# Optimization experiments

Hardware: AMD Instinct MI355X
Metric: run time of the kernel (lower is better)

## Reference

```python
import jax, jax.numpy as jnp
import numpy as np

B, S, D = 16, 1024, 512
H, DH = 8, 64  # heads, dim_head


def setup_inputs() -> dict:
    key = jax.random.key(0)
    ks = jax.random.split(key, 7)
    x = jax.random.normal(ks[0], (B, S, D), dtype=jnp.float32)
    # variable sequence lengths in [1, S]
    seq_lens = jnp.maximum(jax.random.randint(ks[1], (B,), 0, S + 1), 1).astype(jnp.int32)
    w_std = 0.02
    Wq = jax.random.normal(ks[2], (D, D), dtype=jnp.float32) * w_std
    Wk = jax.random.normal(ks[3], (D, D), dtype=jnp.float32) * w_std
    Wv = jax.random.normal(ks[4], (D, D), dtype=jnp.float32) * w_std
    Wo = jax.random.normal(ks[5], (D, D), dtype=jnp.float32) * w_std
    bo = jnp.zeros((D,), dtype=jnp.float32)
    return {"x": x, "seq_lens": seq_lens, "Wq": Wq, "Wk": Wk, "Wv": Wv, "Wo": Wo, "bo": bo}


def reference(x, seq_lens, Wq, Wk, Wv, Wo, bo):
    # x: [B, S, D] padded ragged batch; seq_lens: [B] valid token counts.
    # Equivalent to the per-batch SDPA loop over jagged sequences: attention
    # is computed only among the valid tokens of each sequence.
    scale = DH ** -0.5
    q = (x @ Wq).reshape(B, S, H, DH)
    k = (x @ Wk).reshape(B, S, H, DH)
    v = (x @ Wv).reshape(B, S, H, DH)
    scores = jnp.einsum('bqhd,bkhd->bhqk', q, k) * scale  # [B,H,S,S]
    valid = jnp.arange(S)[None, :] < seq_lens[:, None]     # [B,S] token mask
    neg_inf = jnp.finfo(scores.dtype).min
    scores = jnp.where(valid[:, None, None, :], scores, neg_inf)
    attn = jax.nn.softmax(scores, axis=-1)
    out = jnp.einsum('bhqk,bkhd->bqhd', attn, v).reshape(B, S, D)
    out = out @ Wo + bo  # to_out Linear (dropout=0 / eval)
    return out * valid[:, :, None]  # zero padded query positions
```

## Files before the change

### kernel.cpp

```cpp
#include <hip/hip_runtime.h>
#include <hip/hip_bf16.h>

typedef __bf16 bf16_t;
typedef __attribute__((ext_vector_type(4))) __bf16 bf16x4;
typedef __attribute__((ext_vector_type(8))) __bf16 bf16x8;
typedef __attribute__((ext_vector_type(4))) float f32x4;

#define MFMA16(a, b, c) __builtin_amdgcn_mfma_f32_16x16x32_bf16((a), (b), (c), 0, 0, 0)

#define BB 16
#define SS 1024
#define DD 512
#define HH 8
#define DH 64
#define NTOK (BB * SS)
#define QSCALE 0.18033688f

typedef const __attribute__((address_space(1))) void gas_void;
typedef __attribute__((address_space(3))) void las_void;

__device__ __forceinline__ void async_cp16(const void* g, void* l) {
    __builtin_amdgcn_global_load_lds((gas_void*)g, (las_void*)l, 16, 0, 0);
}

__device__ __forceinline__ bf16x8 frag_ld(const char* sm, int row, int kk, int g) {
    int r7 = row & 7;
    int base = row * 128 + ((g & 1) << 3);
    int c0 = ((kk << 2) + (g >> 1)) ^ r7;
    int c1 = ((kk << 2) + 2 + (g >> 1)) ^ r7;
    bf16x4 lo = *(const bf16x4*)(sm + base + (c0 << 4));
    bf16x4 hi = *(const bf16x4*)(sm + base + (c1 << 4));
    return __builtin_shufflevector(lo, hi, 0, 1, 2, 3, 4, 5, 6, 7);
}

__device__ __forceinline__ bf16x8 fragl(const char* sm, int idx, int l) {
    return *(const bf16x8*)(sm + (idx * 64 + l) * 16);
}

__global__ __launch_bounds__(256) void cast_x_k(const float* __restrict__ x,
                                                bf16_t* __restrict__ xb, int n4) {
    int i = blockIdx.x * 256 + threadIdx.x;
    if (i < n4) {
        float4 v = ((const float4*)x)[i];
        bf16x4 o;
        o[0] = (bf16_t)v.x; o[1] = (bf16_t)v.y; o[2] = (bf16_t)v.z; o[3] = (bf16_t)v.w;
        *(bf16x4*)(xb + (size_t)i * 4) = o;
    }
}

__global__ __launch_bounds__(256) void transpose_w_k(const float* __restrict__ W0,
                                                     const float* __restrict__ W1,
                                                     const float* __restrict__ W2,
                                                     const float* __restrict__ W3,
                                                     bf16_t* __restrict__ Wt) {
    __shared__ float t[32][33];
    int z = blockIdx.z;
    const float* W = (z == 0) ? W0 : (z == 1) ? W1 : (z == 2) ? W2 : W3;
    bf16_t* out = Wt + (size_t)z * DD * DD;
    int n0 = blockIdx.x * 32, k0 = blockIdx.y * 32;
    int tx = threadIdx.x, ty = threadIdx.y;
#pragma unroll
    for (int i = 0; i < 32; i += 8)
        t[ty + i][tx] = W[(size_t)(k0 + ty + i) * DD + n0 + tx];
    __syncthreads();
#pragma unroll
    for (int i = 0; i < 32; i += 8)
        out[(size_t)(n0 + ty + i) * DD + k0 + tx] = (bf16_t)t[tx][ty + i];
}

__global__ void build_q_k(const int* __restrict__ sl, ushort* __restrict__ items,
                          int* __restrict__ meta) {
    int l = threadIdx.x;
    __shared__ int s_b[BB], s_cnt[BB], s_start[BB];
    if (l < BB) {
        int len = sl[l];
        int rank = 0;
        for (int j = 0; j < BB; ++j) {
            int lj = sl[j];
            if (lj > len || (lj == len && j < l)) ++rank;
        }
        s_b[rank] = l;
        s_cnt[rank] = ((len + 63) >> 6) * HH;
    }
    __syncthreads();
    if (l < BB) {
        int st = 0;
        for (int j = 0; j < l; ++j) st += s_cnt[j];
        s_start[l] = st;
        if (l == BB - 1) { meta[0] = st + s_cnt[l]; meta[1] = 0; }
    }
    __syncthreads();
    if (l < BB) {
        int b = s_b[l], st = s_start[l], c = s_cnt[l];
        int nq = c >> 3;
        for (int i = 0; i < c; ++i) {
            int h = i / nq, qt = i - h * nq;
            items[st + i] = (ushort)((((b << 3) | h) << 4) | qt);
        }
    }
}

template <int MODE>
__global__ __launch_bounds__(256) void gemm_k(const bf16_t* __restrict__ A,
                                              const bf16_t* __restrict__ WtBase,
                                              bf16_t* __restrict__ oQ,
                                              bf16_t* __restrict__ oK,
                                              bf16_t* __restrict__ oVt,
                                              float* __restrict__ oO,
                                              const float* __restrict__ bo,
                                              const int* __restrict__ seq_lens) {
    __shared__ __align__(16) char smem[32768];
    char* smA = smem;
    char* smB = smem + 16384;
    const int tid = threadIdx.x;
    const int l = tid & 63, w = tid >> 6;
    const int lr = l & 15, g = l >> 4;
    const int bm = blockIdx.x, bn = blockIdx.y;
    const int z = (MODE == 0) ? blockIdx.z : 3;
    const bf16_t* Wt = WtBase + (size_t)z * DD * DD;
    const int row0 = bm * 128;
    const int col0 = bn * 128;
    const int wm = (w >> 1) * 64, wn = (w & 1) * 64;

    const int bb = row0 >> 10, s0 = row0 & 1023;
    const int len = seq_lens[bb];

    if (MODE == 0) {
        if (s0 >= ((len + 63) & ~63)) return;
    } else {
        if (s0 >= len) {
#pragma unroll
            for (int i = 0; i < 4; ++i) {
                int mrow = row0 + wm + i * 16 + g * 4;
#pragma unroll
                for (int j = 0; j < 4; ++j) {
                    int n = col0 + wn + j * 16 + lr;
#pragma unroll
                    for (int r = 0; r < 4; ++r)
                        oO[(size_t)(mrow + r) * DD + n] = 0.f;
                }
            }
            return;
        }
    }

    f32x4 acc[4][4] = {};

    for (int kt = 0; kt < 8; ++kt) {
        const int k0 = kt * 64;
        __syncthreads();
#pragma unroll
        for (int it = 0; it < 4; ++it) {
            int cl = it * 256 + tid;
            int m = cl >> 3, p = cl & 7, c = p ^ (m & 7);
            async_cp16(A + (size_t)(row0 + m) * DD + k0 + c * 8, smA + cl * 16);
        }
#pragma unroll
        for (int it = 0; it < 4; ++it) {
            int cl = it * 256 + tid;
            int m = cl >> 3, p = cl & 7, c = p ^ (m & 7);
            async_cp16(Wt + (size_t)(col0 + m) * DD + k0 + c * 8, smB + cl * 16);
        }
        __syncthreads();
#pragma unroll
        for (int kk = 0; kk < 2; ++kk) {
            bf16x8 af[4], bfr[4];
#pragma unroll
            for (int i = 0; i < 4; ++i) af[i] = frag_ld(smA, wm + i * 16 + lr, kk, g);
#pragma unroll
            for (int j = 0; j < 4; ++j) bfr[j] = frag_ld(smB, wn + j * 16 + lr, kk, g);
#pragma unroll
            for (int i = 0; i < 4; ++i)
#pragma unroll
                for (int j = 0; j < 4; ++j)
                    acc[i][j] = MFMA16(af[i], bfr[j], acc[i][j]);
        }
    }

    if (MODE == 0) {
        __syncthreads();
        char* tl = smem;
        const float sc = (z == 0) ? QSCALE : 1.f;
#pragma unroll
        for (int i = 0; i < 4; ++i)
#pragma unroll
            for (int j = 0; j < 4; ++j)
#pragma unroll
                for (int r = 0; r < 4; ++r) {
                    int s = wm + i * 16 + g * 4 + r;
                    int n = wn + j * 16 + lr;
                    int nb = 2 * n;
                    int byte = s * 256 + ((((nb >> 4) ^ (s & 7)) << 4) | (nb & 15));
                    *(bf16_t*)(tl + byte) = (bf16_t)(acc[i][j][r] * sc);
                }
        __syncthreads();
        const int b = bb;
        if (z < 2) {
            bf16_t* dst = (z == 0) ? oQ : oK;
#pragma unroll
            for (int c8 = 0; c8 < 8; ++c8) {
                int combo = c8 * 4 + w;
                int kk = combo & 1, t = (combo >> 1) & 7, hl = combo >> 4;
                int s = 16 * t + lr;
                bf16x4 pr[2];
#pragma unroll
                for (int jj = 0; jj < 2; ++jj) {
                    int nb = 128 * hl + 64 * kk + 32 * jj + 8 * g;
                    int byte = s * 256 + ((((nb >> 4) ^ (s & 7)) << 4) | (nb & 15));
                    pr[jj] = *(const bf16x4*)(tl + byte);
                }
                bf16x8 v = __builtin_shufflevector(pr[0], pr[1], 0, 1, 2, 3, 4, 5, 6, 7);
                int bhh = b * 8 + (col0 >> 6) + hl;
                int tg = (s0 >> 4) + t;
                *(bf16x8*)(dst + (((size_t)bhh * 64 + tg) * 2 + kk) * 512 + l * 8) = v;
            }
        } else {
#pragma unroll
            for (int c8 = 0; c8 < 8; ++c8) {
                int combo = c8 * 4 + w;
                int kk = combo & 1, dt = (combo >> 1) & 3;
                int st = (combo >> 3) & 1, hl = (combo >> 4) & 1;
                bf16x8 v;
#pragma unroll
                for (int j = 0; j < 8; ++j) {
                    int s = 64 * st + 32 * kk + 16 * (j >> 2) + 4 * g + (j & 3);
                    int n = 64 * hl + 16 * dt + lr;
                    int nb = 2 * n;
                    int byte = s * 256 + ((((nb >> 4) ^ (s & 7)) << 4) | (nb & 15));
                    v[j] = *(const bf16_t*)(tl + byte);
                }
                int bhh = b * 8 + (col0 >> 6) + hl;
                int stg = (s0 >> 6) + st;
                *(bf16x8*)(oVt + ((((size_t)bhh * 16 + stg) * 4 + dt) * 2 + kk) * 512 +
                           l * 8) = v;
            }
        }
    } else {
        const bool fullv = (s0 + 128 <= len);
#pragma unroll
        for (int i = 0; i < 4; ++i) {
            int mrow = row0 + wm + i * 16 + g * 4;
#pragma unroll
            for (int j = 0; j < 4; ++j) {
                int n = col0 + wn + j * 16 + lr;
                float bias = bo[n];
                if (fullv) {
#pragma unroll
                    for (int r = 0; r < 4; ++r)
                        oO[(size_t)(mrow + r) * DD + n] = acc[i][j][r] + bias;
                } else {
#pragma unroll
                    for (int r = 0; r < 4; ++r) {
                        int m = mrow + r;
                        int s = m & 1023;
                        oO[(size_t)m * DD + n] = (s < len) ? (acc[i][j][r] + bias) : 0.f;
                    }
                }
            }
        }
    }
}

__global__ __launch_bounds__(256) void attn_k(const bf16_t* __restrict__ Qf,
                                              const bf16_t* __restrict__ Kf,
                                              const bf16_t* __restrict__ Vf,
                                              bf16_t* __restrict__ O,
                                              const int* __restrict__ seq_lens,
                                              const ushort* __restrict__ items,
                                              int* __restrict__ meta) {
    __shared__ __align__(16) char smem[32768];
    __shared__ int s_item;
    const int tid = threadIdx.x, l = tid & 63, w = tid >> 6;
    const int lr = l & 15, g = l >> 4;
    const int nitems = meta[0];
    int* cursor = meta + 1;

    for (;;) {
        if (tid == 0) s_item = atomicAdd(cursor, 1);
        __syncthreads();
        const int ii = s_item;
        if (ii >= nitems) return;
        const int itv = items[ii];
        const int qt = itv & 15, bh = itv >> 4;
        const int b = bh >> 3, h = bh & 7;
        const int len = seq_lens[b];
        const int q0 = qt * 64 + w * 16;

        const bf16_t* kfb = Kf + (size_t)bh * 65536;
        const bf16_t* vfb = Vf + (size_t)bh * 65536;

        bf16x8 bq[2];
        {
            size_t tb = ((size_t)bh * 64 + (q0 >> 4)) * 2;
            bq[0] = *(const bf16x8*)(Qf + (tb + 0) * 512 + l * 8);
            bq[1] = *(const bf16x8*)(Qf + (tb + 1) * 512 + l * 8);
        }

        f32x4 oacc[4] = {};
        float mrun = -1e30f, lpart = 0.f;

        const int nkt = (len + 63) >> 6;

        auto stage = [&](int buf, int kti) {
            char* smK = smem + buf * 16384;
            char* smV = smK + 8192;
            const bf16_t* ks = kfb + kti * 4096;
            const bf16_t* vs = vfb + kti * 4096;
            async_cp16(ks + tid * 8, smK + tid * 16);
            async_cp16(ks + (256 + tid) * 8, smK + (256 + tid) * 16);
            async_cp16(vs + tid * 8, smV + tid * 16);
            async_cp16(vs + (256 + tid) * 8, smV + (256 + tid) * 16);
        };

        stage(0, 0);
        int cur = 0;

        for (int kt = 0; kt < nkt; ++kt) {
            const int key0 = kt * 64;
            asm volatile("s_waitcnt vmcnt(0)" ::: "memory");
            __builtin_amdgcn_s_barrier();
            if (kt + 1 < nkt) stage(cur ^ 1, kt + 1);
            const char* smK = smem + cur * 16384;
            const char* smV = smK + 8192;

            f32x4 pacc[4] = {};
            __builtin_amdgcn_s_setprio(1);
#pragma unroll
            for (int nt = 0; nt < 4; ++nt) {
                bf16x8 ak0 = fragl(smK, nt * 2 + 0, l);
                bf16x8 ak1 = fragl(smK, nt * 2 + 1, l);
                pacc[nt] = MFMA16(ak0, bq[0], pacc[nt]);
                pacc[nt] = MFMA16(ak1, bq[1], pacc[nt]);
            }
            __builtin_amdgcn_s_setprio(0);

            const bool full = (key0 + 64 <= len);

            float mloc = -1e30f;
            if (full) {
#pragma unroll
                for (int nt = 0; nt < 4; ++nt)
#pragma unroll
                    for (int r = 0; r < 4; ++r) mloc = fmaxf(mloc, pacc[nt][r]);
            } else {
#pragma unroll
                for (int nt = 0; nt < 4; ++nt)
#pragma unroll
                    for (int r = 0; r < 4; ++r) {
                        int kg = key0 + nt * 16 + 4 * g + r;
                        float s = (kg < len) ? pacc[nt][r] : -1e30f;
                        pacc[nt][r] = s;
                        mloc = fmaxf(mloc, s);
                    }
            }
            mloc = fmaxf(mloc, __shfl_xor(mloc, 16, 64));
            mloc = fmaxf(mloc, __shfl_xor(mloc, 32, 64));

            if (!__all(mloc <= mrun + 8.f)) {
                float mn = fmaxf(mrun, mloc);
                float corr = __builtin_amdgcn_exp2f(mrun - mn);
                mrun = mn;
                lpart *= corr;
                float cb[4];
#pragma unroll
                for (int r = 0; r < 4; ++r) cb[r] = __shfl(corr, 4 * g + r, 64);
#pragma unroll
                for (int dt = 0; dt < 4; ++dt)
#pragma unroll
                    for (int r = 0; r < 4; ++r) oacc[dt][r] *= cb[r];
            }

            float ls = 0.f;
#pragma unroll
            for (int nt = 0; nt < 4; ++nt)
#pragma unroll
                for (int r = 0; r < 4; ++r) {
                    float p = __builtin_amdgcn_exp2f(pacc[nt][r] - mrun);
                    pacc[nt][r] = p;
                    ls += p;
                }
            lpart += ls;

            bf16x8 pa[2];
#pragma unroll
            for (int kf = 0; kf < 2; ++kf)
#pragma unroll
                for (int j = 0; j < 8; ++j)
                    pa[kf][j] = (bf16_t)pacc[2 * kf + (j >> 2)][j & 3];
            __builtin_amdgcn_s_setprio(1);
#pragma unroll
            for (int kf = 0; kf < 2; ++kf)
#pragma unroll
                for (int dt = 0; dt < 4; ++dt) {
                    bf16x8 bv = fragl(smV, dt * 2 + kf, l);
                    oacc[dt] = MFMA16(pa[kf], bv, oacc[dt]);
                }
            __builtin_amdgcn_s_setprio(0);
            cur ^= 1;
        }

        {
            float lt = lpart;
            lt += __shfl_xor(lt, 16, 64);
            lt += __shfl_xor(lt, 32, 64);
#pragma unroll
            for (int r = 0; r < 4; ++r) {
                float inv = 1.f / __shfl(lt, 4 * g + r, 64);
                int q = q0 + 4 * g + r;
                size_t orow = ((size_t)b * SS + q) * DD;
#pragma unroll
                for (int dt = 0; dt < 4; ++dt)
                    O[orow + h * DH + dt * 16 + lr] = (bf16_t)(oacc[dt][r] * inv);
            }
        }
    }
}

extern "C" void kernel_launch(void* const* d_in, const int* in_sizes, int n_in,
                              void* d_out, int out_size, void* d_ws, size_t ws_size,
                              hipStream_t stream) {
    const float* x = (const float*)d_in[0];
    const int* seq_lens = (const int*)d_in[1];
    const float* Wq = (const float*)d_in[2];
    const float* Wk = (const float*)d_in[3];
    const float* Wv = (const float*)d_in[4];
    const float* Wo = (const float*)d_in[5];
    const float* bo = (const float*)d_in[6];
    float* out = (float*)d_out;

    char* ws = (char*)d_ws;
    const size_t SEG = (size_t)NTOK * DD * sizeof(bf16_t);
    bf16_t* xb = (bf16_t*)ws;
    bf16_t* qb = (bf16_t*)(ws + SEG);
    bf16_t* kb = (bf16_t*)(ws + 2 * SEG);
    bf16_t* vtb = (bf16_t*)(ws + 3 * SEG);
    bf16_t* wt = (bf16_t*)(ws + 4 * SEG);
    ushort* items = (ushort*)(ws + 4 * SEG + (size_t)4 * DD * DD * sizeof(bf16_t));
    int* meta = (int*)(items + 4096);
    bf16_t* ab = xb;

    build_q_k<<<dim3(1), dim3(64), 0, stream>>>(seq_lens, items, meta);
    cast_x_k<<<dim3((NTOK * DD / 4) / 256), dim3(256), 0, stream>>>(x, xb, NTOK * DD / 4);
    transpose_w_k<<<dim3(16, 16, 4), dim3(32, 8), 0, stream>>>(Wq, Wk, Wv, Wo, wt);
    gemm_k<0><<<dim3(NTOK / 128, DD / 128, 3), dim3(256), 0, stream>>>(
        xb, wt, qb, kb, vtb, nullptr, nullptr, seq_lens);
    attn_k<<<dim3(1280), dim3(256), 0, stream>>>(qb, kb, vtb, ab, seq_lens, items, meta);
    gemm_k<2><<<dim3(NTOK / 128, DD / 128, 1), dim3(256), 0, stream>>>(
        ab, wt, nullptr, nullptr, nullptr, out, bo, seq_lens);
}
```

Before: 129.0 us.

## Fuse fp32-to-bf16 cast into QKV GEMM and shard attention queue per head

```diff
diff --git a/kernel.cpp b/kernel.cpp
--- a/kernel.cpp
+++ b/kernel.cpp
@@ -35,17 +35,6 @@
 
 __device__ __forceinline__ bf16x8 fragl(const char* sm, int idx, int l) {
     return *(const bf16x8*)(sm + (idx * 64 + l) * 16);
-}
-
-__global__ __launch_bounds__(256) void cast_x_k(const float* __restrict__ x,
-                                                bf16_t* __restrict__ xb, int n4) {
-    int i = blockIdx.x * 256 + threadIdx.x;
-    if (i < n4) {
-        float4 v = ((const float4*)x)[i];
-        bf16x4 o;
-        o[0] = (bf16_t)v.x; o[1] = (bf16_t)v.y; o[2] = (bf16_t)v.z; o[3] = (bf16_t)v.w;
-        *(bf16x4*)(xb + (size_t)i * 4) = o;
-    }
 }
 
 __global__ __launch_bounds__(256) void transpose_w_k(const float* __restrict__ W0,
@@ -80,28 +69,27 @@
             if (lj > len || (lj == len && j < l)) ++rank;
         }
         s_b[rank] = l;
-        s_cnt[rank] = ((len + 63) >> 6) * HH;
+        s_cnt[rank] = (len + 63) >> 6;
     }
     __syncthreads();
     if (l < BB) {
         int st = 0;
         for (int j = 0; j < l; ++j) st += s_cnt[j];
         s_start[l] = st;
-        if (l == BB - 1) { meta[0] = st + s_cnt[l]; meta[1] = 0; }
-    }
+        if (l == BB - 1) meta[0] = st + s_cnt[l];
+    }
+    if (l >= 48 && l < 56) meta[1 + (l - 48)] = 0;
     __syncthreads();
     if (l < BB) {
         int b = s_b[l], st = s_start[l], c = s_cnt[l];
-        int nq = c >> 3;
-        for (int i = 0; i < c; ++i) {
-            int h = i / nq, qt = i - h * nq;
-            items[st + i] = (ushort)((((b << 3) | h) << 4) | qt);
-        }
+        for (int i = 0; i < c; ++i)
+            items[st + i] = (ushort)((b << 4) | i);
     }
 }
 
 template <int MODE>
-__global__ __launch_bounds__(256) void gemm_k(const bf16_t* __restrict__ A,
+__global__ __launch_bounds__(256) void gemm_k(const float* __restrict__ Af,
+                                              const bf16_t* __restrict__ A,
                                               const bf16_t* __restrict__ WtBase,
                                               bf16_t* __restrict__ oQ,
                                               bf16_t* __restrict__ oK,
@@ -149,11 +137,29 @@
     for (int kt = 0; kt < 8; ++kt) {
         const int k0 = kt * 64;
         __syncthreads();
-#pragma unroll
-        for (int it = 0; it < 4; ++it) {
-            int cl = it * 256 + tid;
-            int m = cl >> 3, p = cl & 7, c = p ^ (m & 7);
-            async_cp16(A + (size_t)(row0 + m) * DD + k0 + c * 8, smA + cl * 16);
+        if (MODE == 0) {
+#pragma unroll
+            for (int it = 0; it < 4; ++it) {
+                int cl = it * 256 + tid;
+                int m = cl >> 3, c = cl & 7;
+                const float* src = Af + (size_t)(row0 + m) * DD + k0 + c * 8;
+                float4 f0 = *(const float4*)(src);
+                float4 f1 = *(const float4*)(src + 4);
+                bf16x8 v;
+                v[0] = (bf16_t)f0.x; v[1] = (bf16_t)f0.y;
+                v[2] = (bf16_t)f0.z; v[3] = (bf16_t)f0.w;
+                v[4] = (bf16_t)f1.x; v[5] = (bf16_t)f1.y;
+                v[6] = (bf16_t)f1.z; v[7] = (bf16_t)f1.w;
+                int cs = c ^ (m & 7);
+                *(bf16x8*)(smA + (m * 8 + cs) * 16) = v;
+            }
+        } else {
+#pragma unroll
+            for (int it = 0; it < 4; ++it) {
+                int cl = it * 256 + tid;
+                int m = cl >> 3, p = cl & 7, c = p ^ (m & 7);
+                async_cp16(A + (size_t)(row0 + m) * DD + k0 + c * 8, smA + cl * 16);
+            }
         }
 #pragma unroll
         for (int it = 0; it < 4; ++it) {
@@ -273,7 +279,8 @@
     const int tid = threadIdx.x, l = tid & 63, w = tid >> 6;
     const int lr = l & 15, g = l >> 4;
     const int nitems = meta[0];
-    int* cursor = meta + 1;
+    const int h = blockIdx.x & 7;
+    int* cursor = meta + 1 + h;
 
     for (;;) {
         if (tid == 0) s_item = atomicAdd(cursor, 1);
@@ -281,8 +288,8 @@
         const int ii = s_item;
         if (ii >= nitems) return;
         const int itv = items[ii];
-        const int qt = itv & 15, bh = itv >> 4;
-        const int b = bh >> 3, h = bh & 7;
+        const int qt = itv & 15, b = itv >> 4;
+        const int bh = b * 8 + h;
         const int len = seq_lens[b];
         const int q0 = qt * 64 + w * 16;
 
@@ -324,7 +331,6 @@
             const char* smV = smK + 8192;
 
             f32x4 pacc[4] = {};
-            __builtin_amdgcn_s_setprio(1);
 #pragma unroll
             for (int nt = 0; nt < 4; ++nt) {
                 bf16x8 ak0 = fragl(smK, nt * 2 + 0, l);
@@ -332,7 +338,6 @@
                 pacc[nt] = MFMA16(ak0, bq[0], pacc[nt]);
                 pacc[nt] = MFMA16(ak1, bq[1], pacc[nt]);
             }
-            __builtin_amdgcn_s_setprio(0);
 
             const bool full = (key0 + 64 <= len);
 
@@ -387,7 +392,6 @@
 #pragma unroll
                 for (int j = 0; j < 8; ++j)
                     pa[kf][j] = (bf16_t)pacc[2 * kf + (j >> 2)][j & 3];
-            __builtin_amdgcn_s_setprio(1);
 #pragma unroll
             for (int kf = 0; kf < 2; ++kf)
 #pragma unroll
@@ -395,7 +399,6 @@
                     bf16x8 bv = fragl(smV, dt * 2 + kf, l);
                     oacc[dt] = MFMA16(pa[kf], bv, oacc[dt]);
                 }
-            __builtin_amdgcn_s_setprio(0);
             cur ^= 1;
         }
 
@@ -430,21 +433,19 @@
 
     char* ws = (char*)d_ws;
     const size_t SEG = (size_t)NTOK * DD * sizeof(bf16_t);
-    bf16_t* xb = (bf16_t*)ws;
+    bf16_t* ab = (bf16_t*)ws;
     bf16_t* qb = (bf16_t*)(ws + SEG);
     bf16_t* kb = (bf16_t*)(ws + 2 * SEG);
     bf16_t* vtb = (bf16_t*)(ws + 3 * SEG);
     bf16_t* wt = (bf16_t*)(ws + 4 * SEG);
     ushort* items = (ushort*)(ws + 4 * SEG + (size_t)4 * DD * DD * sizeof(bf16_t));
     int* meta = (int*)(items + 4096);
-    bf16_t* ab = xb;
 
     build_q_k<<<dim3(1), dim3(64), 0, stream>>>(seq_lens, items, meta);
-    cast_x_k<<<dim3((NTOK * DD / 4) / 256), dim3(256), 0, stream>>>(x, xb, NTOK * DD / 4);
     transpose_w_k<<<dim3(16, 16, 4), dim3(32, 8), 0, stream>>>(Wq, Wk, Wv, Wo, wt);
     gemm_k<0><<<dim3(NTOK / 128, DD / 128, 3), dim3(256), 0, stream>>>(
-        xb, wt, qb, kb, vtb, nullptr, nullptr, seq_lens);
+        x, nullptr, wt, qb, kb, vtb, nullptr, nullptr, seq_lens);
     attn_k<<<dim3(1280), dim3(256), 0, stream>>>(qb, kb, vtb, ab, seq_lens, items, meta);
     gemm_k<2><<<dim3(NTOK / 128, DD / 128, 1), dim3(256), 0, stream>>>(
-        ab, wt, nullptr, nullptr, nullptr, out, bo, seq_lens);
-}
+        nullptr, ab, wt, nullptr, nullptr, nullptr, out, bo, seq_lens);
+}
```

Result: no change. 128.9 us (-0.0%).
